# Kernel tuning notes

Hardware: AMD Instinct MI355X
Metric: run time of the kernel (lower is better)

The kernel has to match this reference:

```python
import jax, jax.numpy as jnp
import numpy as np

TEMP = 0.05
EPS = 1e-8  # torch CosineSimilarity eps


def setup_inputs() -> dict:
    key = jax.random.key(0)
    k1, k2 = jax.random.split(key)
    feature1 = jax.random.normal(k1, (4096, 768), dtype=jnp.float32)
    feature2 = jax.random.normal(k2, (4096, 768), dtype=jnp.float32)
    return {"feature1": feature1, "feature2": feature2}


def reference(feature1, feature2):
    # cosine similarity via L2-normalize + GEMM (same math as broadcast cos_sim)
    n1 = feature1 / jnp.maximum(jnp.linalg.norm(feature1, axis=-1, keepdims=True), EPS)
    n2 = feature2 / jnp.maximum(jnp.linalg.norm(feature2, axis=-1, keepdims=True), EPS)
    logits = jnp.einsum("id,jd->ij", n1, n2) / TEMP  # [N, N]
    # cross-entropy with labels = arange(N) -> mean of -log_softmax diagonal
    logp = jax.nn.log_softmax(logits, axis=-1)
    loss = -jnp.mean(jnp.diagonal(logp))
    return loss
```

## Files before the change

kernel.cpp:

```cpp
#include <hip/hip_runtime.h>
#include <hip/hip_bf16.h>

#define NROWS 4096
#define DIM   768
#define NKT   12

typedef __attribute__((ext_vector_type(8))) short short8;
typedef __attribute__((ext_vector_type(4))) float f32x4;

#define GAS(p) ((const __attribute__((address_space(1))) void*)(p))
#define SAS(p) ((__attribute__((address_space(3))) void*)(p))

__device__ __forceinline__ unsigned short f2bf(float x) {
    unsigned int u = __builtin_bit_cast(unsigned int, x);
    u += 0x7fffu + ((u >> 16) & 1u);
    return (unsigned short)(u >> 16);
}

__global__ __launch_bounds__(256) void k_norm(const float* __restrict__ f1,
                                              const float* __restrict__ f2,
                                              unsigned short* __restrict__ n1,
                                              unsigned short* __restrict__ n2,
                                              float* __restrict__ rowsum) {
    int b = blockIdx.x;
    int wid = threadIdx.x >> 6, lane = threadIdx.x & 63;
    int rowidx = b * 4 + wid;
    const float* src = (rowidx < NROWS) ? f1 : f2;
    unsigned short* dst = (rowidx < NROWS) ? n1 : n2;
    int row = rowidx & (NROWS - 1);
    const float4* srow = (const float4*)(src + (size_t)row * DIM);
    float4 v[3];
    float ss = 0.f;
#pragma unroll
    for (int r = 0; r < 3; ++r) {
        v[r] = srow[lane + 64 * r];
        ss += v[r].x * v[r].x + v[r].y * v[r].y + v[r].z * v[r].z + v[r].w * v[r].w;
    }
#pragma unroll
    for (int off = 32; off; off >>= 1) ss += __shfl_xor(ss, off);
    float inv = 1.0f / fmaxf(sqrtf(ss), 1e-8f);
    ushort4* drow = (ushort4*)(dst + (size_t)row * DIM);
#pragma unroll
    for (int r = 0; r < 3; ++r) {
        ushort4 o;
        o.x = f2bf(v[r].x * inv);
        o.y = f2bf(v[r].y * inv);
        o.z = f2bf(v[r].z * inv);
        o.w = f2bf(v[r].w * inv);
        drow[lane + 64 * r] = o;
    }
    if (b == 0) {
        float4 z = {0.f, 0.f, 0.f, 0.f};
#pragma unroll
        for (int i = 0; i < 4; ++i) ((float4*)rowsum)[threadIdx.x + 256 * i] = z;
    }
}


#define BARRIER __builtin_amdgcn_s_barrier()
#define WAIT_LGKM0 do { asm volatile("s_waitcnt lgkmcnt(0)" ::: "memory"); \
                        __builtin_amdgcn_sched_barrier(0); } while (0)
#define WAIT_VM4   do { asm volatile("s_waitcnt vmcnt(4)" ::: "memory"); \
                        __builtin_amdgcn_sched_barrier(0); } while (0)
#define PRIO1 __builtin_amdgcn_s_setprio(1)
#define PRIO0 __builtin_amdgcn_s_setprio(0)

__global__ __launch_bounds__(512, 2) void k_gemm_lse(const unsigned short* __restrict__ n1,
                                                     const unsigned short* __restrict__ n2,
                                                     float* __restrict__ rowsum,
                                                     float* __restrict__ diag) {
    __shared__ alignas(16) char ldsbuf[131072];
    char* ldsc = (char*)ldsbuf;

    int wg = blockIdx.x;
    int swz = (wg & 7) * 32 + (wg >> 3);
    int bi = swz >> 4;
    int bj = swz & 15;

    int tid = threadIdx.x;
    int wid = tid >> 6;
    int lane = tid & 63;
    int l15 = lane & 15, lk = lane >> 4;
    int wr = wid >> 2, wc = wid & 3;

    const unsigned short* abase = n1 + (size_t)bi * 256 * DIM;
    const unsigned short* bbase = n2 + (size_t)bj * 256 * DIM;

    const int stoff = (tid >> 3) * DIM + (((tid & 7) ^ ((tid >> 3) & 7)) * 8);

    const int swzl = (lane & 7) << 4;
    const int lko0 = l15 * 128 + ((lk * 16) ^ swzl);
    const int lko1 = l15 * 128 + (((64 + lk * 16)) ^ swzl);

    char* LA[2];
    char* LB[2];
    LA[0] = ldsc + (0 * 4 + wr) * 16384;
    LA[1] = ldsc + (1 * 4 + wr) * 16384;
    LB[0] = ldsc + (0 * 4 + 2 + (wc >> 1)) * 16384 + (wc & 1) * (64 * 128);
    LB[1] = ldsc + (1 * 4 + 2 + (wc >> 1)) * 16384 + (wc & 1) * (64 * 128);

#define STG(b, slot, base, half, kt) do { \
    const unsigned short* _s = (base) + ((half) * 128) * DIM + (kt) * 64 + stoff; \
    char* _d = ldsc + ((b) * 4 + (slot)) * 16384 + wid * 1024; \
    __builtin_amdgcn_global_load_lds(GAS(_s), SAS(_d), 16, 0, 0); \
    __builtin_amdgcn_global_load_lds(GAS(_s + 64 * DIM), SAS(_d + 8192), 16, 0, 0); \
} while (0)

#define LDA_(b, qm, areg) do { _Pragma("unroll") for (int m = 0; m < 4; ++m) { \
    const char* _p = LA[b] + ((qm) * 64 + m * 16) * 128; \
    areg[m][0] = *(const short8*)(_p + lko0); \
    areg[m][1] = *(const short8*)(_p + lko1); } } while (0)

#define LDB_(b, qn, breg) do { _Pragma("unroll") for (int n = 0; n < 2; ++n) { \
    const char* _p = LB[b] + ((qn) * 2 + n) * 16 * 128; \
    breg[n][0] = *(const short8*)(_p + lko0); \
    breg[n][1] = *(const short8*)(_p + lko1); } } while (0)

#define MM_(qm, qn, areg, breg) do { _Pragma("unroll") for (int m = 0; m < 4; ++m) \
    _Pragma("unroll") for (int n = 0; n < 2; ++n) { \
    f32x4* _c = &acc[(qm) * 4 + m][(qn) * 2 + n]; \
    *_c = __builtin_amdgcn_mfma_f32_16x16x32_bf16(areg[m][0], breg[n][0], *_c, 0, 0, 0); \
    *_c = __builtin_amdgcn_mfma_f32_16x16x32_bf16(areg[m][1], breg[n][1], *_c, 0, 0, 0); } } while (0)

    short8 aA[4][2], aB[4][2], b0[2][2], b1[2][2];
    f32x4 acc[8][4] = {};

    STG(0, 0, abase, 0, 0); STG(0, 1, abase, 1, 0);
    STG(0, 2, bbase, 0, 0); STG(0, 3, bbase, 1, 0);
    STG(1, 2, bbase, 0, 1); STG(1, 3, bbase, 1, 1);
    WAIT_VM4;
    BARRIER;
    LDA_(0, 0, aA); LDB_(0, 0, b0);

    for (int t = 0; t < NKT; t += 2) {
        int t1 = t + 1;
        int t2 = (t + 2 < NKT) ? t + 2 : t + 2 - NKT;
        int t3 = (t + 3 < NKT) ? t + 3 : t + 3 - NKT;
        STG(1, 0, abase, 0, t1);
        BARRIER; WAIT_LGKM0;
        LDB_(0, 1, b1);
        PRIO1; MM_(0, 0, aA, b0); PRIO0;
        BARRIER;
        STG(1, 1, abase, 1, t1);
        BARRIER; WAIT_LGKM0;
        LDA_(0, 1, aB);
        PRIO1; MM_(0, 1, aA, b1); PRIO0;
        BARRIER;
        STG(0, 2, bbase, 0, t2);
        BARRIER; WAIT_LGKM0;
        PRIO1; MM_(1, 1, aB, b1); PRIO0;
        BARRIER;
        STG(0, 3, bbase, 1, t2);
        BARRIER;
        PRIO1; MM_(1, 0, aB, b0); PRIO0;
        WAIT_VM4;
        LDA_(1, 0, aA); LDB_(1, 0, b0);
        BARRIER;
        STG(0, 0, abase, 0, t2);
        BARRIER; WAIT_LGKM0;
        LDB_(1, 1, b1);
        PRIO1; MM_(0, 0, aA, b0); PRIO0;
        BARRIER;
        STG(0, 1, abase, 1, t2);
        BARRIER; WAIT_LGKM0;
        LDA_(1, 1, aB);
        PRIO1; MM_(0, 1, aA, b1); PRIO0;
        BARRIER;
        STG(1, 2, bbase, 0, t3);
        BARRIER; WAIT_LGKM0;
        PRIO1; MM_(1, 1, aB, b1); PRIO0;
        BARRIER;
        STG(1, 3, bbase, 1, t3);
        BARRIER;
        PRIO1; MM_(1, 0, aB, b0); PRIO0;
        WAIT_VM4;
        LDA_(0, 0, aA); LDB_(0, 0, b0);
        BARRIER;
    }

    __syncthreads();

    const bool dblk = (bi == bj);
    const int rowb = bi * 256 + wr * 128;
    const int colb = bj * 256 + wc * 64;
#pragma unroll
    for (int mi = 0; mi < 8; ++mi) {
#pragma unroll
        for (int r = 0; r < 4; ++r) {
            float s = 0.f;
            int gi = rowb + mi * 16 + lk * 4 + r;
#pragma unroll
            for (int ni = 0; ni < 4; ++ni) {
                float v = acc[mi][ni][r] * 20.0f;
                s += __expf(v);
                if (dblk) {
                    int gj = colb + ni * 16 + l15;
                    if (gi == gj) diag[gi] = v;
                }
            }
#pragma unroll
            for (int off = 1; off < 16; off <<= 1) s += __shfl_xor(s, off);
            if (l15 == 0) atomicAdd(rowsum + gi, s);
        }
    }
}

__global__ __launch_bounds__(1024) void k_final(const float* __restrict__ rowsum,
                                                const float* __restrict__ diag,
                                                float* __restrict__ out) {
    int tid = threadIdx.x;
    float s = 0.f;
#pragma unroll
    for (int i = 0; i < 4; ++i) {
        int idx = tid + 1024 * i;
        s += logf(rowsum[idx]) - diag[idx];
    }
#pragma unroll
    for (int off = 32; off; off >>= 1) s += __shfl_xor(s, off);
    __shared__ float red[16];
    if ((tid & 63) == 0) red[tid >> 6] = s;
    __syncthreads();
    if (tid == 0) {
        float tot = 0.f;
#pragma unroll
        for (int i = 0; i < 16; ++i) tot += red[i];
        out[0] = tot * (1.0f / NROWS);
    }
}

extern "C" void kernel_launch(void* const* d_in, const int* in_sizes, int n_in,
                              void* d_out, int out_size, void* d_ws, size_t ws_size,
                              hipStream_t stream) {
    const float* f1 = (const float*)d_in[0];
    const float* f2 = (const float*)d_in[1];
    float* out = (float*)d_out;

    char* ws = (char*)d_ws;
    unsigned short* n1 = (unsigned short*)ws;
    unsigned short* n2 = n1 + (size_t)NROWS * DIM;
    float* rowsum = (float*)(ws + 2 * (size_t)NROWS * DIM * sizeof(unsigned short));
    float* diag = rowsum + NROWS;

    k_norm<<<2048, 256, 0, stream>>>(f1, f2, n1, n2, rowsum);
    k_gemm_lse<<<256, 512, 0, stream>>>(n1, n2, rowsum, diag);
    k_final<<<1, 1024, 0, stream>>>(rowsum, diag, out);
}
```

Baseline: 106.3 us.

## Shrink GEMM tiles to 128x128 with 4 waves and a simpler double-buffer pipeline

Replaces the 256x256 output tile per 512-thread workgroup with a 128x128 tile per 256-thread workgroup, launching 1024 workgroups instead of 256. LDS drops to 64KB, so two workgroups can share a CU, and the k-loop becomes a simpler two-stage double buffer that stages a whole k-slice at once and waits with vmcnt(8). The aim is better CU occupancy and fewer barriers on a 256-CU part, at the cost of lower operand reuse per tile, which roughly doubles global and LDS traffic per FLOP.

New measurement: 113.0 us. +6.4%, slower.

```diff
diff --git a/kernel.cpp b/kernel.cpp
--- a/kernel.cpp
+++ b/kernel.cpp
@@ -60,31 +60,31 @@
 #define BARRIER __builtin_amdgcn_s_barrier()
 #define WAIT_LGKM0 do { asm volatile("s_waitcnt lgkmcnt(0)" ::: "memory"); \
                         __builtin_amdgcn_sched_barrier(0); } while (0)
-#define WAIT_VM4   do { asm volatile("s_waitcnt vmcnt(4)" ::: "memory"); \
+#define WAIT_VM8   do { asm volatile("s_waitcnt vmcnt(8)" ::: "memory"); \
                         __builtin_amdgcn_sched_barrier(0); } while (0)
 #define PRIO1 __builtin_amdgcn_s_setprio(1)
 #define PRIO0 __builtin_amdgcn_s_setprio(0)
 
-__global__ __launch_bounds__(512, 2) void k_gemm_lse(const unsigned short* __restrict__ n1,
+__global__ __launch_bounds__(256, 2) void k_gemm_lse(const unsigned short* __restrict__ n1,
                                                      const unsigned short* __restrict__ n2,
                                                      float* __restrict__ rowsum,
                                                      float* __restrict__ diag) {
-    __shared__ alignas(16) char ldsbuf[131072];
+    __shared__ alignas(16) char ldsbuf[65536];
     char* ldsc = (char*)ldsbuf;
 
     int wg = blockIdx.x;
-    int swz = (wg & 7) * 32 + (wg >> 3);
-    int bi = swz >> 4;
-    int bj = swz & 15;
+    int swz = (wg & 7) * 128 + (wg >> 3);
+    int bi = swz >> 5;
+    int bj = swz & 31;
 
     int tid = threadIdx.x;
     int wid = tid >> 6;
     int lane = tid & 63;
     int l15 = lane & 15, lk = lane >> 4;
-    int wr = wid >> 2, wc = wid & 3;
-
-    const unsigned short* abase = n1 + (size_t)bi * 256 * DIM;
-    const unsigned short* bbase = n2 + (size_t)bj * 256 * DIM;
+    int wr = wid >> 1, wc = wid & 1;
+
+    const unsigned short* abase = n1 + (size_t)bi * 128 * DIM;
+    const unsigned short* bbase = n2 + (size_t)bj * 128 * DIM;
 
     const int stoff = (tid >> 3) * DIM + (((tid & 7) ^ ((tid >> 3) & 7)) * 8);
 
@@ -92,99 +92,79 @@
     const int lko0 = l15 * 128 + ((lk * 16) ^ swzl);
     const int lko1 = l15 * 128 + (((64 + lk * 16)) ^ swzl);
 
-    char* LA[2];
-    char* LB[2];
-    LA[0] = ldsc + (0 * 4 + wr) * 16384;
-    LA[1] = ldsc + (1 * 4 + wr) * 16384;
-    LB[0] = ldsc + (0 * 4 + 2 + (wc >> 1)) * 16384 + (wc & 1) * (64 * 128);
-    LB[1] = ldsc + (1 * 4 + 2 + (wc >> 1)) * 16384 + (wc & 1) * (64 * 128);
-
-#define STG(b, slot, base, half, kt) do { \
-    const unsigned short* _s = (base) + ((half) * 128) * DIM + (kt) * 64 + stoff; \
-    char* _d = ldsc + ((b) * 4 + (slot)) * 16384 + wid * 1024; \
+    char* LAp[2] = { ldsc + wr * 8192,          ldsc + 32768 + wr * 8192 };
+    char* LBp[2] = { ldsc + 16384 + wc * 8192,  ldsc + 32768 + 16384 + wc * 8192 };
+
+#define STG1(b, isB, base, chunk, kt) do { \
+    const unsigned short* _s = (base) + ((chunk) * 32) * DIM + (kt) * 64 + stoff; \
+    char* _d = ldsc + (b) * 32768 + (isB) * 16384 + (chunk) * 4096 + tid * 16; \
     __builtin_amdgcn_global_load_lds(GAS(_s), SAS(_d), 16, 0, 0); \
-    __builtin_amdgcn_global_load_lds(GAS(_s + 64 * DIM), SAS(_d + 8192), 16, 0, 0); \
 } while (0)
 
-#define LDA_(b, qm, areg) do { _Pragma("unroll") for (int m = 0; m < 4; ++m) { \
-    const char* _p = LA[b] + ((qm) * 64 + m * 16) * 128; \
+#define STG8(b, kt) do { \
+    STG1(b, 0, abase, 0, kt); STG1(b, 0, abase, 1, kt); \
+    STG1(b, 0, abase, 2, kt); STG1(b, 0, abase, 3, kt); \
+    STG1(b, 1, bbase, 0, kt); STG1(b, 1, bbase, 1, kt); \
+    STG1(b, 1, bbase, 2, kt); STG1(b, 1, bbase, 3, kt); \
+} while (0)
+
+#define LDA2(b, q, areg) do { _Pragma("unroll") for (int m = 0; m < 2; ++m) { \
+    const char* _p = LAp[b] + ((q) * 32 + m * 16) * 128; \
     areg[m][0] = *(const short8*)(_p + lko0); \
     areg[m][1] = *(const short8*)(_p + lko1); } } while (0)
 
-#define LDB_(b, qn, breg) do { _Pragma("unroll") for (int n = 0; n < 2; ++n) { \
-    const char* _p = LB[b] + ((qn) * 2 + n) * 16 * 128; \
+#define LDB4(b, breg) do { _Pragma("unroll") for (int n = 0; n < 4; ++n) { \
+    const char* _p = LBp[b] + n * 16 * 128; \
     breg[n][0] = *(const short8*)(_p + lko0); \
     breg[n][1] = *(const short8*)(_p + lko1); } } while (0)
 
-#define MM_(qm, qn, areg, breg) do { _Pragma("unroll") for (int m = 0; m < 4; ++m) \
-    _Pragma("unroll") for (int n = 0; n < 2; ++n) { \
-    f32x4* _c = &acc[(qm) * 4 + m][(qn) * 2 + n]; \
+#define MMH(qm, areg, breg) do { _Pragma("unroll") for (int m = 0; m < 2; ++m) \
+    _Pragma("unroll") for (int n = 0; n < 4; ++n) { \
+    f32x4* _c = &acc[(qm) * 2 + m][n]; \
     *_c = __builtin_amdgcn_mfma_f32_16x16x32_bf16(areg[m][0], breg[n][0], *_c, 0, 0, 0); \
     *_c = __builtin_amdgcn_mfma_f32_16x16x32_bf16(areg[m][1], breg[n][1], *_c, 0, 0, 0); } } while (0)
 
-    short8 aA[4][2], aB[4][2], b0[2][2], b1[2][2];
-    f32x4 acc[8][4] = {};
-
-    STG(0, 0, abase, 0, 0); STG(0, 1, abase, 1, 0);
-    STG(0, 2, bbase, 0, 0); STG(0, 3, bbase, 1, 0);
-    STG(1, 2, bbase, 0, 1); STG(1, 3, bbase, 1, 1);
-    WAIT_VM4;
+    short8 a0A[2][2], a1A[2][2], aB[2][2], b0[4][2], b1[4][2];
+    f32x4 acc[4][4] = {};
+
+    STG8(0, 0);
+    STG8(1, 1);
+    WAIT_VM8;
     BARRIER;
-    LDA_(0, 0, aA); LDB_(0, 0, b0);
+    LDA2(0, 0, a0A); LDB4(0, b0);
 
     for (int t = 0; t < NKT; t += 2) {
-        int t1 = t + 1;
         int t2 = (t + 2 < NKT) ? t + 2 : t + 2 - NKT;
         int t3 = (t + 3 < NKT) ? t + 3 : t + 3 - NKT;
-        STG(1, 0, abase, 0, t1);
-        BARRIER; WAIT_LGKM0;
-        LDB_(0, 1, b1);
-        PRIO1; MM_(0, 0, aA, b0); PRIO0;
-        BARRIER;
-        STG(1, 1, abase, 1, t1);
-        BARRIER; WAIT_LGKM0;
-        LDA_(0, 1, aB);
-        PRIO1; MM_(0, 1, aA, b1); PRIO0;
-        BARRIER;
-        STG(0, 2, bbase, 0, t2);
-        BARRIER; WAIT_LGKM0;
-        PRIO1; MM_(1, 1, aB, b1); PRIO0;
-        BARRIER;
-        STG(0, 3, bbase, 1, t2);
-        BARRIER;
-        PRIO1; MM_(1, 0, aB, b0); PRIO0;
-        WAIT_VM4;
-        LDA_(1, 0, aA); LDB_(1, 0, b0);
-        BARRIER;
-        STG(0, 0, abase, 0, t2);
-        BARRIER; WAIT_LGKM0;
-        LDB_(1, 1, b1);
-        PRIO1; MM_(0, 0, aA, b0); PRIO0;
-        BARRIER;
-        STG(0, 1, abase, 1, t2);
-        BARRIER; WAIT_LGKM0;
-        LDA_(1, 1, aB);
-        PRIO1; MM_(0, 1, aA, b1); PRIO0;
-        BARRIER;
-        STG(1, 2, bbase, 0, t3);
-        BARRIER; WAIT_LGKM0;
-        PRIO1; MM_(1, 1, aB, b1); PRIO0;
-        BARRIER;
-        STG(1, 3, bbase, 1, t3);
-        BARRIER;
-        PRIO1; MM_(1, 0, aB, b0); PRIO0;
-        WAIT_VM4;
-        LDA_(0, 0, aA); LDB_(0, 0, b0);
+        WAIT_LGKM0;
+        LDA2(0, 1, aB);
+        PRIO1; MMH(0, a0A, b0); PRIO0;
+        WAIT_LGKM0;
+        BARRIER;
+        STG8(0, t2);
+        PRIO1; MMH(1, aB, b0); PRIO0;
+        WAIT_VM8;
+        LDA2(1, 0, a1A); LDB4(1, b1);
+        BARRIER;
+        WAIT_LGKM0;
+        LDA2(1, 1, aB);
+        PRIO1; MMH(0, a1A, b1); PRIO0;
+        WAIT_LGKM0;
+        BARRIER;
+        STG8(1, t3);
+        PRIO1; MMH(1, aB, b1); PRIO0;
+        WAIT_VM8;
+        LDA2(0, 0, a0A); LDB4(0, b0);
         BARRIER;
     }
 
     __syncthreads();
 
     const bool dblk = (bi == bj);
-    const int rowb = bi * 256 + wr * 128;
-    const int colb = bj * 256 + wc * 64;
-#pragma unroll
-    for (int mi = 0; mi < 8; ++mi) {
+    const int rowb = bi * 128 + wr * 64;
+    const int colb = bj * 128 + wc * 64;
+#pragma unroll
+    for (int mi = 0; mi < 4; ++mi) {
 #pragma unroll
         for (int r = 0; r < 4; ++r) {
             float s = 0.f;
@@ -242,6 +222,6 @@
     float* diag = rowsum + NROWS;
 
     k_norm<<<2048, 256, 0, stream>>>(f1, f2, n1, n2, rowsum);
-    k_gemm_lse<<<256, 512, 0, stream>>>(n1, n2, rowsum, diag);
+    k_gemm_lse<<<1024, 256, 0, stream>>>(n1, n2, rowsum, diag);
     k_final<<<1, 1024, 0, stream>>>(rowsum, diag, out);
 }
```
